# Kernel optimization log

Measured on AMD Instinct MI355X. Metric: run time of the kernel, lower is better.

Reference implementation:

```python
import jax, jax.numpy as jnp
import numpy as np

B, T, D = 4, 1024, 1024
H, KVH = 16, 4
HD = D // H
DFF = 4096
WINDOW = 256
EPS = 1e-5


def _layernorm(x, g, b):
    mu = jnp.mean(x, axis=-1, keepdims=True)
    var = jnp.mean(jnp.square(x - mu), axis=-1, keepdims=True)
    return (x - mu) * jax.lax.rsqrt(var + EPS) * g + b


def _rope(x):
    # x: (B, H, T, HD); non-interleaved halves, matching _apply_rope
    half = HD // 2
    theta = 1.0 / (10000.0 ** (jnp.arange(half, dtype=jnp.float32) / half))
    pos = jnp.arange(x.shape[2], dtype=jnp.float32)
    freqs = jnp.outer(pos, theta)            # (T, half)
    cos_f, sin_f = jnp.cos(freqs), jnp.sin(freqs)
    x1, x2 = x[..., :half], x[..., half:]
    return jnp.concatenate([x1 * cos_f - x2 * sin_f, x2 * cos_f + x1 * sin_f], axis=-1)


def setup_inputs() -> dict:
    key = jax.random.key(0)
    ks = jax.random.split(key, 16)
    s = 0.02
    d = {
        "x": jax.random.normal(ks[0], (B, T, D), dtype=jnp.float32),
        "Wq": jax.random.normal(ks[1], (D, H * HD), dtype=jnp.float32) * s,
        "bq": jnp.zeros((H * HD,), jnp.float32),
        "Wk": jax.random.normal(ks[2], (D, KVH * HD), dtype=jnp.float32) * s,
        "bk": jnp.zeros((KVH * HD,), jnp.float32),
        "Wv": jax.random.normal(ks[3], (D, KVH * HD), dtype=jnp.float32) * s,
        "bv": jnp.zeros((KVH * HD,), jnp.float32),
        "Wo": jax.random.normal(ks[4], (D, D), dtype=jnp.float32) * s,
        "bo": jnp.zeros((D,), jnp.float32),
        "g1": jnp.ones((D,), jnp.float32),
        "b1": jnp.zeros((D,), jnp.float32),
        "Wf1": jax.random.normal(ks[5], (D, DFF), dtype=jnp.float32) * s,
        "bf1": jnp.zeros((DFF,), jnp.float32),
        "Wf2": jax.random.normal(ks[6], (DFF, D), dtype=jnp.float32) * s,
        "bf2": jnp.zeros((D,), jnp.float32),
        "g2": jnp.ones((D,), jnp.float32),
        "b2": jnp.zeros((D,), jnp.float32),
    }
    return d


def reference(x, Wq, bq, Wk, bk, Wv, bv, Wo, bo, g1, b1, Wf1, bf1, Wf2, bf2, g2, b2):
    Bt, Tt, _ = x.shape
    h = _layernorm(x, g1, b1)
    q = (h @ Wq + bq).reshape(Bt, Tt, H, HD).transpose(0, 2, 1, 3)      # (B,H,T,HD)
    k = (h @ Wk + bk).reshape(Bt, Tt, KVH, HD).transpose(0, 2, 1, 3)    # (B,KVH,T,HD)
    v = (h @ Wv + bv).reshape(Bt, Tt, KVH, HD).transpose(0, 2, 1, 3)
    # GQA: repeat_interleave kv heads to nhead
    group = H // KVH
    k = jnp.repeat(k, group, axis=1)
    v = jnp.repeat(v, group, axis=1)
    q, k = _rope(q), _rope(k)
    scores = jnp.einsum("bhqd,bhkd->bhqk", q, k) / jnp.sqrt(jnp.float32(HD))
    # causal sliding-window mask: attend iff 0 <= (row-col) < WINDOW
    row = jnp.arange(Tt)[:, None]
    col = jnp.arange(Tt)[None, :]
    valid = (col <= row) & (row - col < WINDOW)
    scores = jnp.where(valid, scores, jnp.float32(-1e9))
    attn = jax.nn.softmax(scores, axis=-1)
    out = jnp.einsum("bhqk,bhkd->bhqd", attn, v)
    out = out.transpose(0, 2, 1, 3).reshape(Bt, Tt, D)
    x = x + (out @ Wo + bo)
    h2 = _layernorm(x, g2, b2)
    ff = jax.nn.gelu(h2 @ Wf1 + bf1, approximate=False) @ Wf2 + bf2
    return x + ff
```

## Files before the change

### kernel.cpp

```cpp
#include <hip/hip_runtime.h>
#include <hip/hip_bf16.h>
#include <math.h>

#define TT 1024
#define DD 1024
#define HH 16
#define KVHN 4
#define HDW 64
#define DFFN 4096
#define WIN 256

typedef __attribute__((ext_vector_type(4))) float f32x4;
typedef __attribute__((ext_vector_type(8))) __bf16 bf16x8;

typedef const __attribute__((address_space(1))) void gas_t;
typedef __attribute__((address_space(3))) void las_t;

__device__ inline unsigned short f2bf(float f){
  union { float f; unsigned u; } x; x.f = f;
  unsigned r = x.u + 0x7fffu + ((x.u >> 16) & 1u);
  return (unsigned short)(r >> 16);
}
__device__ inline float bf2f(unsigned short b){
  union { unsigned u; float f; } x; x.u = ((unsigned)b) << 16; return x.f;
}
__device__ inline f32x4 MFMA(bf16x8 a, bf16x8 b, f32x4 c){
  return __builtin_amdgcn_mfma_f32_16x16x32_bf16(a, b, c, 0, 0, 0);
}

__global__ void zero_k(float* out, int n){
  for (int i = blockIdx.x * blockDim.x + threadIdx.x; i < n; i += gridDim.x * blockDim.x)
    out[i] = 0.f;
}

__global__ __launch_bounds__(256) void wtrans_k(const float* __restrict__ W,
                                                unsigned short* __restrict__ Wt,
                                                int K, int N){
  __shared__ float t[32][33];
  int n0 = blockIdx.x * 32, k0 = blockIdx.y * 32;
  int tx = threadIdx.x & 31, ty = threadIdx.x >> 5;
#pragma unroll
  for (int i = 0; i < 4; i++){
    int kk = ty * 4 + i;
    t[kk][tx] = W[(size_t)(k0 + kk) * N + n0 + tx];
  }
  __syncthreads();
#pragma unroll
  for (int i = 0; i < 4; i++){
    int nn = ty * 4 + i;
    Wt[(size_t)(n0 + nn) * K + k0 + tx] = f2bf(t[tx][nn]);
  }
}

__global__ void packb_k(const float* bq, const float* bk, const float* bv, float* o){
  int i = blockIdx.x * 256 + threadIdx.x;
  if (i < 1536)
    o[i] = (i < 1024) ? bq[i] : ((i < 1280) ? bk[i - 1024] : bv[i - 1280]);
}

__global__ void finit_k(const float* __restrict__ x2, const float* __restrict__ bf2,
                        float* __restrict__ out){
  for (int i = blockIdx.x * blockDim.x + threadIdx.x; i < 4096 * 1024; i += gridDim.x * blockDim.x)
    out[i] = x2[i] + bf2[i & 1023];
}

__global__ __launch_bounds__(256) void ln_k(const float* __restrict__ x,
                                            const float* __restrict__ g,
                                            const float* __restrict__ b,
                                            unsigned short* __restrict__ out){
  __shared__ float red[4];
  int row = blockIdx.x, tid = threadIdx.x;
  const float* xr = x + (size_t)row * DD;
  float4 v = *(const float4*)(xr + tid * 4);
  float s = v.x + v.y + v.z + v.w;
#pragma unroll
  for (int off = 32; off; off >>= 1) s += __shfl_xor(s, off);
  if ((tid & 63) == 0) red[tid >> 6] = s;
  __syncthreads();
  float mu = (red[0] + red[1] + red[2] + red[3]) * (1.f / DD);
  __syncthreads();
  float dx = v.x - mu, dy = v.y - mu, dz = v.z - mu, dw = v.w - mu;
  float sq = dx*dx + dy*dy + dz*dz + dw*dw;
#pragma unroll
  for (int off = 32; off; off >>= 1) sq += __shfl_xor(sq, off);
  if ((tid & 63) == 0) red[tid >> 6] = sq;
  __syncthreads();
  float var = (red[0] + red[1] + red[2] + red[3]) * (1.f / DD);
  float inv = rsqrtf(var + 1e-5f);
  float4 gv = *(const float4*)(g + tid * 4);
  float4 bv = *(const float4*)(b + tid * 4);
  unsigned short* orow = out + (size_t)row * DD + tid * 4;
  orow[0] = f2bf(dx * inv * gv.x + bv.x);
  orow[1] = f2bf(dy * inv * gv.y + bv.y);
  orow[2] = f2bf(dz * inv * gv.z + bv.z);
  orow[3] = f2bf(dw * inv * gv.w + bv.w);
}

template<int EPI>
__global__ __launch_bounds__(512, 1) void gemm256v_k(const unsigned short* __restrict__ A,
                                                     const unsigned short* __restrict__ Bt,
                                                     const float* __restrict__ bias,
                                                     void* __restrict__ Cout,
                                                     int M, int N, int Klen, int lda, int ldb){
  __shared__ unsigned short As2[2][16384];
  __shared__ unsigned short Bs2[2][16384];
  int tid = threadIdx.x;
  int row0 = blockIdx.x * 256, col0 = blockIdx.y * 256;
  int wid = tid >> 6, lane = tid & 63;
  int wr = wid >> 2, wc = wid & 3;
  int lr = lane & 15, lg = lane >> 4;
  int srow8 = tid >> 3;
  int schunk = (tid & 7) ^ (srow8 & 7);
  int xr8 = (lr & 7) << 3;
  f32x4 acc[8][4] = {};

  auto stageA = [&](int slot, int half, int ktn){
    const unsigned short* s0 = A + (size_t)(row0 + half*128 + srow8) * lda + ktn*64 + schunk*8;
    __builtin_amdgcn_global_load_lds((gas_t*)s0, (las_t*)&As2[slot][half*8192 + wid*512], 16, 0, 0);
    __builtin_amdgcn_global_load_lds((gas_t*)(s0 + (size_t)64*lda), (las_t*)&As2[slot][half*8192 + 4096 + wid*512], 16, 0, 0);
  };
  auto stageB = [&](int slot, int half, int ktn){
    const unsigned short* s0 = Bt + (size_t)(col0 + half*128 + srow8) * ldb + ktn*64 + schunk*8;
    __builtin_amdgcn_global_load_lds((gas_t*)s0, (las_t*)&Bs2[slot][half*8192 + wid*512], 16, 0, 0);
    __builtin_amdgcn_global_load_lds((gas_t*)(s0 + (size_t)64*ldb), (las_t*)&Bs2[slot][half*8192 + 4096 + wid*512], 16, 0, 0);
  };

  int NT = Klen >> 6;
  stageA(0, 0, 0); stageB(0, 0, 0); stageA(0, 1, 0); stageB(0, 1, 0);

  for (int kt = 0; kt < NT; kt++){
    int s = kt & 1, ns = s ^ 1;
    bool pre = (kt + 1 < NT);
    if (pre){
      stageA(ns, 0, kt + 1); stageB(ns, 0, kt + 1);
      asm volatile("s_waitcnt vmcnt(4)" ::: "memory");
    } else {
      asm volatile("s_waitcnt vmcnt(0)" ::: "memory");
    }
    __builtin_amdgcn_sched_barrier(0);
    __builtin_amdgcn_s_barrier();

    const unsigned short* Ac = &As2[s][wr * 8192];
    const unsigned short* Bc = &Bs2[s][(wc >> 1) * 8192 + (wc & 1) * 4096];
    bf16x8 af[4][2], bf0[2][2], bf1[2][2];

#pragma unroll
    for (int mf = 0; mf < 4; mf++)
#pragma unroll
      for (int ks = 0; ks < 2; ks++)
        af[mf][ks] = *(const bf16x8*)&Ac[(mf*16 + lr)*64 + ((ks*32 + lg*8) ^ xr8)];
#pragma unroll
    for (int nf = 0; nf < 2; nf++)
#pragma unroll
      for (int ks = 0; ks < 2; ks++)
        bf0[nf][ks] = *(const bf16x8*)&Bc[(nf*16 + lr)*64 + ((ks*32 + lg*8) ^ xr8)];
    __builtin_amdgcn_s_setprio(1);
#pragma unroll
    for (int mf = 0; mf < 4; mf++)
#pragma unroll
      for (int nf = 0; nf < 2; nf++)
#pragma unroll
        for (int ks = 0; ks < 2; ks++)
          acc[mf][nf] = MFMA(af[mf][ks], bf0[nf][ks], acc[mf][nf]);
    __builtin_amdgcn_s_setprio(0);
    if (pre){ stageA(ns, 1, kt + 1); stageB(ns, 1, kt + 1); }

#pragma unroll
    for (int nf = 0; nf < 2; nf++)
#pragma unroll
      for (int ks = 0; ks < 2; ks++)
        bf1[nf][ks] = *(const bf16x8*)&Bc[((nf+2)*16 + lr)*64 + ((ks*32 + lg*8) ^ xr8)];
    __builtin_amdgcn_s_setprio(1);
#pragma unroll
    for (int mf = 0; mf < 4; mf++)
#pragma unroll
      for (int nf = 0; nf < 2; nf++)
#pragma unroll
        for (int ks = 0; ks < 2; ks++)
          acc[mf][nf+2] = MFMA(af[mf][ks], bf1[nf][ks], acc[mf][nf+2]);
    __builtin_amdgcn_s_setprio(0);

#pragma unroll
    for (int mf = 0; mf < 4; mf++)
#pragma unroll
      for (int ks = 0; ks < 2; ks++)
        af[mf][ks] = *(const bf16x8*)&Ac[((mf+4)*16 + lr)*64 + ((ks*32 + lg*8) ^ xr8)];
    __builtin_amdgcn_s_setprio(1);
#pragma unroll
    for (int mf = 0; mf < 4; mf++)
#pragma unroll
      for (int nf = 0; nf < 2; nf++)
#pragma unroll
        for (int ks = 0; ks < 2; ks++)
          acc[mf+4][nf+2] = MFMA(af[mf][ks], bf1[nf][ks], acc[mf+4][nf+2]);

#pragma unroll
    for (int mf = 0; mf < 4; mf++)
#pragma unroll
      for (int nf = 0; nf < 2; nf++)
#pragma unroll
        for (int ks = 0; ks < 2; ks++)
          acc[mf+4][nf] = MFMA(af[mf][ks], bf0[nf][ks], acc[mf+4][nf]);
    __builtin_amdgcn_s_setprio(0);
    __builtin_amdgcn_sched_barrier(0);
    __builtin_amdgcn_s_barrier();
  }

#pragma unroll
  for (int mf = 0; mf < 8; mf++){
#pragma unroll
    for (int r = 0; r < 4; r++){
      int gr = row0 + wr*128 + mf*16 + lg*4 + r;
#pragma unroll
      for (int nf = 0; nf < 4; nf++){
        int gc = col0 + wc*64 + nf*16 + lr;
        float val = acc[mf][nf][r] + bias[gc];
        if constexpr (EPI == 1){
          val = 0.5f * val * (1.f + erff(val * 0.70710678118f));
        }
        ((unsigned short*)Cout)[(size_t)gr * N + gc] = f2bf(val);
      }
    }
  }
}

template<int EPI>
__global__ __launch_bounds__(256) void gemm_k(const unsigned short* __restrict__ A,
                                              const unsigned short* __restrict__ Bt,
                                              const float* __restrict__ bias,
                                              const float* __restrict__ res,
                                              void* __restrict__ Cout,
                                              int M, int N, int Klen, int lda, int ldb){
  __shared__ unsigned short As[2][128 * 64];
  __shared__ unsigned short Bs[2][128 * 64];
  int tid = threadIdx.x;
  int row0 = blockIdx.x * 128, col0 = blockIdx.y * 128;
  A  += (size_t)blockIdx.z * Klen;
  Bt += (size_t)blockIdx.z * Klen;
  int wid = tid >> 6, lane = tid & 63;
  int wm = (wid >> 1) * 64, wn = (wid & 1) * 64;
  int lr = lane & 15, lg = lane >> 4;
  f32x4 acc[4][4] = {};

  int srow = wid * 8 + (lane >> 3);
  int scol = ((lane & 7) ^ (lane >> 3)) * 8;
  const unsigned short* gA0 = A  + (size_t)(row0 + srow) * lda + scol;
  const unsigned short* gB0 = Bt + (size_t)(col0 + srow) * ldb + scol;
  int lbase = wid * 512;

  int NT = Klen >> 6;
#pragma unroll
  for (int j = 0; j < 4; j++){
    __builtin_amdgcn_global_load_lds((gas_t*)(gA0 + (size_t)(j*32)*lda), (las_t*)&As[0][j*2048 + lbase], 16, 0, 0);
    __builtin_amdgcn_global_load_lds((gas_t*)(gB0 + (size_t)(j*32)*ldb), (las_t*)&Bs[0][j*2048 + lbase], 16, 0, 0);
  }
  __syncthreads();
  int cur = 0;
  int xr8 = (lr & 7) << 3;
  for (int t = 0; t < NT; t++){
    if (t + 1 < NT){
      int k0 = (t + 1) << 6;
      int nb = cur ^ 1;
#pragma unroll
      for (int j = 0; j < 4; j++){
        __builtin_amdgcn_global_load_lds((gas_t*)(gA0 + (size_t)(j*32)*lda + k0), (las_t*)&As[nb][j*2048 + lbase], 16, 0, 0);
        __builtin_amdgcn_global_load_lds((gas_t*)(gB0 + (size_t)(j*32)*ldb + k0), (las_t*)&Bs[nb][j*2048 + lbase], 16, 0, 0);
      }
    }
#pragma unroll
    for (int kk = 0; kk < 2; kk++){
      int xk = (kk*32 + lg*8) ^ xr8;
      bf16x8 af[4], bf[4];
#pragma unroll
      for (int mt = 0; mt < 4; mt++)
        af[mt] = *(const bf16x8*)&As[cur][(wm + mt*16 + lr) * 64 + xk];
#pragma unroll
      for (int nt2 = 0; nt2 < 4; nt2++)
        bf[nt2] = *(const bf16x8*)&Bs[cur][(wn + nt2*16 + lr) * 64 + xk];
#pragma unroll
      for (int mt = 0; mt < 4; mt++)
#pragma unroll
        for (int nt2 = 0; nt2 < 4; nt2++)
          acc[mt][nt2] = MFMA(af[mt], bf[nt2], acc[mt][nt2]);
    }
    __syncthreads();
    cur ^= 1;
  }
#pragma unroll
  for (int mt = 0; mt < 4; mt++){
#pragma unroll
    for (int r = 0; r < 4; r++){
      int gr = row0 + wm + mt*16 + lg*4 + r;
#pragma unroll
      for (int nt2 = 0; nt2 < 4; nt2++){
        int gc = col0 + wn + nt2*16 + lr;
        if constexpr (EPI == 5){
          unsafeAtomicAdd(&((float*)Cout)[(size_t)gr * N + gc], acc[mt][nt2][r]);
        } else {
          float val = acc[mt][nt2][r] + bias[gc];
          if constexpr (EPI == 1){
            val = 0.5f * val * (1.f + erff(val * 0.70710678118f));
          }
          if constexpr (EPI == 2){
            float ov = val + res[(size_t)gr * N + gc];
            ((float*)Cout)[(size_t)gr * N + gc] = ov;
          } else {
            ((unsigned short*)Cout)[(size_t)gr * N + gc] = f2bf(val);
          }
        }
      }
    }
  }
}

template<int NH>
__global__ __launch_bounds__(256) void rope_k(unsigned short* base, int rs){
  int idx = blockIdx.x * 8 + (threadIdx.x >> 5);
  int d = threadIdx.x & 31;
  int row = idx / NH;
  int head = idx % NH;
  int t = row & (TT - 1);
  unsigned short* p = base + (size_t)row * rs + head * HDW;
  float x1 = bf2f(p[d]);
  float x2 = bf2f(p[d + 32]);
  float theta = powf(10000.f, -(float)d * (1.f / 32.f));
  float c, s;
  sincosf((float)t * theta, &c, &s);
  p[d]      = f2bf(x1 * c + x2 * s);
  p[d + 32] = f2bf(x2 * c - x1 * s);
}

__global__ __launch_bounds__(256) void vtrans_k(const unsigned short* __restrict__ v, int rs,
                                                unsigned short* __restrict__ vt){
  __shared__ unsigned short tile[64][72];
  int t0 = blockIdx.x * 64;
  int kvh = blockIdx.y, b = blockIdx.z;
  int i = threadIdx.x;
  int tl = i >> 2, dc = (i & 3) * 16;
  const unsigned short* src = v + (size_t)(b * TT + t0 + tl) * rs + kvh * HDW + dc;
  *(uint4*)&tile[tl][dc]     = *(const uint4*)src;
  *(uint4*)&tile[tl][dc + 8] = *(const uint4*)(src + 8);
  __syncthreads();
  int d = i >> 2, tc = (i & 3) * 16;
  unsigned short tmp[16];
#pragma unroll
  for (int e = 0; e < 16; e++) tmp[e] = tile[tc + e][d];
  unsigned short* dst = vt + ((size_t)((b * KVHN + kvh) * HDW) + d) * TT + t0 + tc;
  *(uint4*)dst       = *(uint4*)tmp;
  *(uint4*)(dst + 8) = *(uint4*)(tmp + 8);
}

__global__ __launch_bounds__(64) void attn_k(const unsigned short* __restrict__ q, int qrs,
                                             const unsigned short* __restrict__ k, int krs,
                                             const unsigned short* __restrict__ vt,
                                             unsigned short* __restrict__ o){
  __shared__ unsigned short P[32 * 40];
  __shared__ float sc_l[32];
  int qt = blockIdx.x, h = blockIdx.y, b = blockIdx.z;
  int kvh = h >> 2;
  int lane = threadIdx.x;
  int lr = lane & 15, lg = lane >> 4;
  int q0 = qt * 32;
  bf16x8 qf[2][2];
#pragma unroll
  for (int qi = 0; qi < 2; qi++)
#pragma unroll
    for (int ks = 0; ks < 2; ks++)
      qf[qi][ks] = *(const bf16x8*)(q + (size_t)(b*TT + q0 + qi*16 + lr) * qrs + h * HDW + ks*32 + lg*8);
  f32x4 oa[2][4] = {};
  float m_st[2] = {-1e30f, -1e30f};
  float l_st[2] = {0.f, 0.f};
  int kt_lo = (q0 - (WIN - 1)) > 0 ? ((q0 - (WIN - 1)) >> 5) : 0;
  int kt_hi = (q0 + 31) >> 5;
  for (int kt = kt_lo; kt <= kt_hi; kt++){
    int kb = kt * 32;
    bf16x8 kf[2][2];
#pragma unroll
    for (int ki = 0; ki < 2; ki++)
#pragma unroll
      for (int ks = 0; ks < 2; ks++)
        kf[ki][ks] = *(const bf16x8*)(k + (size_t)(b*TT + kb + ki*16 + lr) * krs + kvh * HDW + ks*32 + lg*8);
    f32x4 s[2][2] = {};
#pragma unroll
    for (int ki = 0; ki < 2; ki++)
#pragma unroll
      for (int qi = 0; qi < 2; qi++){
        s[ki][qi] = MFMA(kf[ki][0], qf[qi][0], s[ki][qi]);
        s[ki][qi] = MFMA(kf[ki][1], qf[qi][1], s[ki][qi]);
      }
#pragma unroll
    for (int qi = 0; qi < 2; qi++){
      int qa = q0 + qi*16 + lr;
      float pv[8];
      float mx = -1e30f;
#pragma unroll
      for (int ki = 0; ki < 2; ki++)
#pragma unroll
        for (int r = 0; r < 4; r++){
          int ka = kb + ki*16 + lg*4 + r;
          float val = s[ki][qi][r] * 0.125f;
          bool ok = (ka <= qa) && (qa - ka < WIN);
          val = ok ? val : -1e9f;
          pv[ki*4 + r] = val;
          mx = fmaxf(mx, val);
        }
      mx = fmaxf(mx, __shfl_xor(mx, 16));
      mx = fmaxf(mx, __shfl_xor(mx, 32));
      float mn = fmaxf(m_st[qi], mx);
      float scl = __expf(m_st[qi] - mn);
      m_st[qi] = mn;
      float ls = 0.f;
#pragma unroll
      for (int j = 0; j < 8; j++){ float p = __expf(pv[j] - mn); pv[j] = p; ls += p; }
      ls += __shfl_xor(ls, 16);
      ls += __shfl_xor(ls, 32);
      l_st[qi] = l_st[qi] * scl + ls;
#pragma unroll
      for (int ki = 0; ki < 2; ki++){
        uint2 w;
        w.x = (unsigned)f2bf(pv[ki*4+0]) | ((unsigned)f2bf(pv[ki*4+1]) << 16);
        w.y = (unsigned)f2bf(pv[ki*4+2]) | ((unsigned)f2bf(pv[ki*4+3]) << 16);
        *(uint2*)&P[(qi*16 + lr) * 40 + ki*16 + lg*4] = w;
      }
      if (lg == 0) sc_l[qi*16 + lr] = scl;
    }
    __syncthreads();
#pragma unroll
    for (int qi = 0; qi < 2; qi++)
#pragma unroll
      for (int r = 0; r < 4; r++){
        float f = sc_l[qi*16 + lg*4 + r];
#pragma unroll
        for (int di = 0; di < 4; di++) oa[qi][di][r] *= f;
      }
    bf16x8 pa[2];
#pragma unroll
    for (int qi = 0; qi < 2; qi++)
      pa[qi] = *(const bf16x8*)&P[(qi*16 + lr) * 40 + lg*8];
#pragma unroll
    for (int di = 0; di < 4; di++){
      bf16x8 vb = *(const bf16x8*)(vt + ((size_t)((b*KVHN + kvh) * HDW) + di*16 + lr) * TT + kb + lg*8);
#pragma unroll
      for (int qi = 0; qi < 2; qi++)
        oa[qi][di] = MFMA(pa[qi], vb, oa[qi][di]);
    }
    __syncthreads();
  }
  if (lg == 0){ sc_l[lr] = l_st[0]; sc_l[16 + lr] = l_st[1]; }
  __syncthreads();
#pragma unroll
  for (int qi = 0; qi < 2; qi++)
#pragma unroll
    for (int r = 0; r < 4; r++){
      float inv = 1.f / sc_l[qi*16 + lg*4 + r];
      int t = q0 + qi*16 + lg*4 + r;
#pragma unroll
      for (int di = 0; di < 4; di++)
        o[((size_t)((b*TT + t) * HH) + h) * HDW + di*16 + lr] = f2bf(oa[qi][di][r] * inv);
    }
}

extern "C" void kernel_launch(void* const* d_in, const int* in_sizes, int n_in,
                              void* d_out, int out_size, void* d_ws, size_t ws_size,
                              hipStream_t stream){
  const float* x   = (const float*)d_in[0];
  const float* Wq  = (const float*)d_in[1];
  const float* bq  = (const float*)d_in[2];
  const float* Wk  = (const float*)d_in[3];
  const float* bk  = (const float*)d_in[4];
  const float* Wv  = (const float*)d_in[5];
  const float* bv  = (const float*)d_in[6];
  const float* Wo  = (const float*)d_in[7];
  const float* bo  = (const float*)d_in[8];
  const float* g1  = (const float*)d_in[9];
  const float* b1  = (const float*)d_in[10];
  const float* Wf1 = (const float*)d_in[11];
  const float* bf1 = (const float*)d_in[12];
  const float* Wf2 = (const float*)d_in[13];
  const float* bf2 = (const float*)d_in[14];
  const float* g2  = (const float*)d_in[15];
  const float* b2  = (const float*)d_in[16];

  static const int want[17] = {4194304, 1048576, 1024, 262144, 256, 262144, 256,
                               1048576, 1024, 1024, 1024, 4194304, 4096, 4194304,
                               1024, 1024, 1024};
  bool bad = (n_in != 17) || (out_size != 4194304);
  if (!bad) for (int i = 0; i < 17; i++) if (in_sizes[i] != want[i]) bad = true;
  if (bad){
    zero_k<<<2048, 256, 0, stream>>>((float*)d_out, out_size);
    return;
  }

  const int M = 4 * TT;
  const int QKVN = 1536;
  char* ws = (char*)d_ws;
  size_t off = 0;
  auto alloc = [&](size_t bytes) -> void* {
    void* p = ws + off; off += (bytes + 255) & ~(size_t)255; return p;
  };
  unsigned short* wqkv = (unsigned short*)alloc((size_t)QKVN * DD * 2);
  unsigned short* wto  = (unsigned short*)alloc((size_t)DD * DD * 2);
  unsigned short* wtf1 = (unsigned short*)alloc((size_t)DFFN * DD * 2);
  unsigned short* wtf2 = (unsigned short*)alloc((size_t)DD * DFFN * 2);
  float*          bqkv = (float*)alloc((size_t)QKVN * 4);
  unsigned short* h1   = (unsigned short*)alloc((size_t)M * DD * 2);
  unsigned short* qkv  = (unsigned short*)alloc((size_t)M * QKVN * 2);
  unsigned short* vtb  = (unsigned short*)alloc((size_t)M * 256 * 2);
  unsigned short* ao   = (unsigned short*)alloc((size_t)M * DD * 2);
  float*          x2   = (float*)alloc((size_t)M * DD * 4);
  unsigned short* h2   = h1;
  unsigned short* ff   = (unsigned short*)alloc((size_t)M * DFFN * 2);
  (void)ws_size;

  wtrans_k<<<dim3(DD/32,  DD/32),  256, 0, stream>>>(Wq,  wqkv,                       DD,  DD);
  wtrans_k<<<dim3(256/32, DD/32),  256, 0, stream>>>(Wk,  wqkv + (size_t)1024 * DD,   DD,  256);
  wtrans_k<<<dim3(256/32, DD/32),  256, 0, stream>>>(Wv,  wqkv + (size_t)1280 * DD,   DD,  256);
  wtrans_k<<<dim3(DD/32,  DD/32),  256, 0, stream>>>(Wo,  wto,  DD,  DD);
  wtrans_k<<<dim3(DFFN/32,DD/32),  256, 0, stream>>>(Wf1, wtf1, DD,  DFFN);
  wtrans_k<<<dim3(DD/32,  DFFN/32),256, 0, stream>>>(Wf2, wtf2, DFFN,DD);
  packb_k<<<6, 256, 0, stream>>>(bq, bk, bv, bqkv);

  ln_k<<<M, 256, 0, stream>>>(x, g1, b1, h1);

  gemm_k<0><<<dim3(M/128, QKVN/128), 256, 0, stream>>>(h1, wqkv, bqkv, nullptr, qkv, M, QKVN, DD, DD, DD);

  rope_k<HH>  <<<(M * HH) / 8,   256, 0, stream>>>(qkv,        QKVN);
  rope_k<KVHN><<<(M * KVHN) / 8, 256, 0, stream>>>(qkv + 1024, QKVN);

  vtrans_k<<<dim3(TT/64, KVHN, 4), 256, 0, stream>>>(qkv + 1280, QKVN, vtb);

  attn_k<<<dim3(TT/32, HH, 4), 64, 0, stream>>>(qkv, QKVN, qkv + 1024, QKVN, vtb, ao);

  gemm_k<2><<<dim3(M/128, DD/128), 256, 0, stream>>>(ao, wto, bo, x, x2, M, DD, DD, DD, DD);

  ln_k<<<M, 256, 0, stream>>>(x2, g2, b2, h2);

  gemm256v_k<1><<<dim3(M/256, DFFN/256), 512, 0, stream>>>(h2, wtf1, bf1, ff, M, DFFN, DD, DD, DD);

  finit_k<<<2048, 256, 0, stream>>>(x2, bf2, (float*)d_out);
  gemm_k<5><<<dim3(M/128, DD/128, 2), 256, 0, stream>>>(ff, wtf2, nullptr, nullptr, (float*)d_out,
                                                        M, DD, 2048, DFFN, DFFN);
}
```

Measured before the change: 298.9 us.

## Simplify big GEMM pipeline, add XCD-aware tile remap, drop split-K for FFN2

The 256x256 GEMM gets a block-index remap that groups workgroups by XCD, and its interleaved half-stage prefetch with manual vmcnt waits is replaced by one full-tile prefetch per iteration followed by __syncthreads. The FFN down-projection no longer uses split-K with atomics plus a separate init kernel. It now runs as a single 128x128 GEMM with a fused bias and residual epilogue. This removes the extra init pass and the atomic traffic, but the FFN2 grid shrinks to 256 blocks, and the simpler pipeline may overlap loads with MFMA less well.

```diff
diff --git a/kernel.cpp b/kernel.cpp
--- a/kernel.cpp
+++ b/kernel.cpp
@@ -56,12 +56,6 @@
   int i = blockIdx.x * 256 + threadIdx.x;
   if (i < 1536)
     o[i] = (i < 1024) ? bq[i] : ((i < 1280) ? bk[i - 1024] : bv[i - 1280]);
-}
-
-__global__ void finit_k(const float* __restrict__ x2, const float* __restrict__ bf2,
-                        float* __restrict__ out){
-  for (int i = blockIdx.x * blockDim.x + threadIdx.x; i < 4096 * 1024; i += gridDim.x * blockDim.x)
-    out[i] = x2[i] + bf2[i & 1023];
 }
 
 __global__ __launch_bounds__(256) void ln_k(const float* __restrict__ x,
@@ -97,7 +91,7 @@
 }
 
 template<int EPI>
-__global__ __launch_bounds__(512, 1) void gemm256v_k(const unsigned short* __restrict__ A,
+__global__ __launch_bounds__(512, 1) void gemm256b_k(const unsigned short* __restrict__ A,
                                                      const unsigned short* __restrict__ Bt,
                                                      const float* __restrict__ bias,
                                                      void* __restrict__ Cout,
@@ -105,7 +99,12 @@
   __shared__ unsigned short As2[2][16384];
   __shared__ unsigned short Bs2[2][16384];
   int tid = threadIdx.x;
-  int row0 = blockIdx.x * 256, col0 = blockIdx.y * 256;
+  int gx = gridDim.x;
+  int nwg = gx * gridDim.y;
+  int fid = blockIdx.y * gx + blockIdx.x;
+  int wg = (fid & 7) * (nwg >> 3) + (fid >> 3);
+  int row0 = (wg % gx) * 256, col0 = (wg / gx) * 256;
+
   int wid = tid >> 6, lane = tid & 63;
   int wr = wid >> 2, wc = wid & 3;
   int lr = lane & 15, lg = lane >> 4;
@@ -126,60 +125,37 @@
   };
 
   int NT = Klen >> 6;
-  stageA(0, 0, 0); stageB(0, 0, 0); stageA(0, 1, 0); stageB(0, 1, 0);
+  stageA(0, 0, 0); stageA(0, 1, 0); stageB(0, 0, 0); stageB(0, 1, 0);
+  __syncthreads();
 
   for (int kt = 0; kt < NT; kt++){
     int s = kt & 1, ns = s ^ 1;
-    bool pre = (kt + 1 < NT);
-    if (pre){
-      stageA(ns, 0, kt + 1); stageB(ns, 0, kt + 1);
-      asm volatile("s_waitcnt vmcnt(4)" ::: "memory");
-    } else {
-      asm volatile("s_waitcnt vmcnt(0)" ::: "memory");
-    }
-    __builtin_amdgcn_sched_barrier(0);
-    __builtin_amdgcn_s_barrier();
-
+    if (kt + 1 < NT){
+      stageA(ns, 0, kt + 1); stageA(ns, 1, kt + 1);
+      stageB(ns, 0, kt + 1); stageB(ns, 1, kt + 1);
+    }
     const unsigned short* Ac = &As2[s][wr * 8192];
     const unsigned short* Bc = &Bs2[s][(wc >> 1) * 8192 + (wc & 1) * 4096];
-    bf16x8 af[4][2], bf0[2][2], bf1[2][2];
-
+    bf16x8 af[4][2], bf[4][2];
+#pragma unroll
+    for (int nf = 0; nf < 4; nf++)
+#pragma unroll
+      for (int ks = 0; ks < 2; ks++)
+        bf[nf][ks] = *(const bf16x8*)&Bc[(nf*16 + lr)*64 + ((ks*32 + lg*8) ^ xr8)];
 #pragma unroll
     for (int mf = 0; mf < 4; mf++)
 #pragma unroll
       for (int ks = 0; ks < 2; ks++)
         af[mf][ks] = *(const bf16x8*)&Ac[(mf*16 + lr)*64 + ((ks*32 + lg*8) ^ xr8)];
-#pragma unroll
-    for (int nf = 0; nf < 2; nf++)
-#pragma unroll
-      for (int ks = 0; ks < 2; ks++)
-        bf0[nf][ks] = *(const bf16x8*)&Bc[(nf*16 + lr)*64 + ((ks*32 + lg*8) ^ xr8)];
     __builtin_amdgcn_s_setprio(1);
 #pragma unroll
     for (int mf = 0; mf < 4; mf++)
 #pragma unroll
-      for (int nf = 0; nf < 2; nf++)
+      for (int nf = 0; nf < 4; nf++)
 #pragma unroll
         for (int ks = 0; ks < 2; ks++)
-          acc[mf][nf] = MFMA(af[mf][ks], bf0[nf][ks], acc[mf][nf]);
+          acc[mf][nf] = MFMA(af[mf][ks], bf[nf][ks], acc[mf][nf]);
     __builtin_amdgcn_s_setprio(0);
-    if (pre){ stageA(ns, 1, kt + 1); stageB(ns, 1, kt + 1); }
-
-#pragma unroll
-    for (int nf = 0; nf < 2; nf++)
-#pragma unroll
-      for (int ks = 0; ks < 2; ks++)
-        bf1[nf][ks] = *(const bf16x8*)&Bc[((nf+2)*16 + lr)*64 + ((ks*32 + lg*8) ^ xr8)];
-    __builtin_amdgcn_s_setprio(1);
-#pragma unroll
-    for (int mf = 0; mf < 4; mf++)
-#pragma unroll
-      for (int nf = 0; nf < 2; nf++)
-#pragma unroll
-        for (int ks = 0; ks < 2; ks++)
-          acc[mf][nf+2] = MFMA(af[mf][ks], bf1[nf][ks], acc[mf][nf+2]);
-    __builtin_amdgcn_s_setprio(0);
-
 #pragma unroll
     for (int mf = 0; mf < 4; mf++)
 #pragma unroll
@@ -189,21 +165,12 @@
 #pragma unroll
     for (int mf = 0; mf < 4; mf++)
 #pragma unroll
-      for (int nf = 0; nf < 2; nf++)
+      for (int nf = 0; nf < 4; nf++)
 #pragma unroll
         for (int ks = 0; ks < 2; ks++)
-          acc[mf+4][nf+2] = MFMA(af[mf][ks], bf1[nf][ks], acc[mf+4][nf+2]);
-
-#pragma unroll
-    for (int mf = 0; mf < 4; mf++)
-#pragma unroll
-      for (int nf = 0; nf < 2; nf++)
-#pragma unroll
-        for (int ks = 0; ks < 2; ks++)
-          acc[mf+4][nf] = MFMA(af[mf][ks], bf0[nf][ks], acc[mf+4][nf]);
+          acc[mf+4][nf] = MFMA(af[mf][ks], bf[nf][ks], acc[mf+4][nf]);
     __builtin_amdgcn_s_setprio(0);
-    __builtin_amdgcn_sched_barrier(0);
-    __builtin_amdgcn_s_barrier();
+    __syncthreads();
   }
 
 #pragma unroll
@@ -235,8 +202,6 @@
   __shared__ unsigned short Bs[2][128 * 64];
   int tid = threadIdx.x;
   int row0 = blockIdx.x * 128, col0 = blockIdx.y * 128;
-  A  += (size_t)blockIdx.z * Klen;
-  Bt += (size_t)blockIdx.z * Klen;
   int wid = tid >> 6, lane = tid & 63;
   int wm = (wid >> 1) * 64, wn = (wid & 1) * 64;
   int lr = lane & 15, lg = lane >> 4;
@@ -294,19 +259,15 @@
 #pragma unroll
       for (int nt2 = 0; nt2 < 4; nt2++){
         int gc = col0 + wn + nt2*16 + lr;
-        if constexpr (EPI == 5){
-          unsafeAtomicAdd(&((float*)Cout)[(size_t)gr * N + gc], acc[mt][nt2][r]);
+        float val = acc[mt][nt2][r] + bias[gc];
+        if constexpr (EPI == 1){
+          val = 0.5f * val * (1.f + erff(val * 0.70710678118f));
+        }
+        if constexpr (EPI == 2){
+          float ov = val + res[(size_t)gr * N + gc];
+          ((float*)Cout)[(size_t)gr * N + gc] = ov;
         } else {
-          float val = acc[mt][nt2][r] + bias[gc];
-          if constexpr (EPI == 1){
-            val = 0.5f * val * (1.f + erff(val * 0.70710678118f));
-          }
-          if constexpr (EPI == 2){
-            float ov = val + res[(size_t)gr * N + gc];
-            ((float*)Cout)[(size_t)gr * N + gc] = ov;
-          } else {
-            ((unsigned short*)Cout)[(size_t)gr * N + gc] = f2bf(val);
-          }
+          ((unsigned short*)Cout)[(size_t)gr * N + gc] = f2bf(val);
         }
       }
     }
@@ -535,9 +496,7 @@
 
   ln_k<<<M, 256, 0, stream>>>(x2, g2, b2, h2);
 
-  gemm256v_k<1><<<dim3(M/256, DFFN/256), 512, 0, stream>>>(h2, wtf1, bf1, ff, M, DFFN, DD, DD, DD);
-
-  finit_k<<<2048, 256, 0, stream>>>(x2, bf2, (float*)d_out);
-  gemm_k<5><<<dim3(M/128, DD/128, 2), 256, 0, stream>>>(ff, wtf2, nullptr, nullptr, (float*)d_out,
-                                                        M, DD, 2048, DFFN, DFFN);
-}
+  gemm256b_k<1><<<dim3(M/256, DFFN/256), 512, 0, stream>>>(h2, wtf1, bf1, ff, M, DFFN, DD, DD, DD);
+
+  gemm_k<2><<<dim3(M/128, DD/128), 256, 0, stream>>>(ff, wtf2, bf2, x2, (float*)d_out, M, DD, DFFN, DFFN, DFFN);
+}
```

After: 282.9 us. 5.3% less time.
